# Kernel tuning notes

Hardware: AMD Instinct MI355X
Metric: run time of the kernel (lower is better)

## Reference

```python
import jax, jax.numpy as jnp
import numpy as np

N, E, D, L = 50000, 600000, 128, 3
EPS = 1e-5


def _layer_norm(x, g, b):
    m = jnp.mean(x, axis=-1, keepdims=True)
    v = jnp.mean((x - m) ** 2, axis=-1, keepdims=True)
    return (x - m) * jax.lax.rsqrt(v + EPS) * g + b


def setup_inputs() -> dict:
    key = jax.random.key(0)
    ks = jax.random.split(key, 20)
    s = 1.0 / np.sqrt(D)
    inp = {
        "node": jax.random.normal(ks[0], (N, D), jnp.float32),
        "edge_attr": jax.random.uniform(ks[1], (E,), jnp.float32),
        # stacked per-layer parameters [L, ...]
        "W_rel": jax.random.uniform(ks[2], (L, D, D), jnp.float32, -s, s),
        "b_rel": jax.random.uniform(ks[3], (L, D), jnp.float32, -s, s),
        "W_root": jax.random.uniform(ks[4], (L, D, D), jnp.float32, -s, s),
        "ln1_g": jnp.ones((L, D), jnp.float32),
        "ln1_b": jnp.zeros((L, D), jnp.float32),
        "ln2_g": jnp.ones((L, D), jnp.float32),
        "ln2_b": jnp.zeros((L, D), jnp.float32),
        "W1": jax.random.uniform(ks[5], (L, D, D), jnp.float32, -s, s),
        "b1": jax.random.uniform(ks[6], (L, D), jnp.float32, -s, s),
        "W2": jax.random.uniform(ks[7], (L, D, D), jnp.float32, -s, s),
        "b2": jax.random.uniform(ks[8], (L, D), jnp.float32, -s, s),
        "jk_W": jax.random.uniform(ks[9], (L * D, D), jnp.float32, -1.0 / np.sqrt(L * D), 1.0 / np.sqrt(L * D)),
        "jk_b": jax.random.uniform(ks[10], (D,), jnp.float32, -1.0 / np.sqrt(L * D), 1.0 / np.sqrt(L * D)),
        "edge_index": jax.random.randint(ks[11], (2, E), 0, N, jnp.int64),
        "batch_ptr": jnp.sort(jax.random.randint(ks[12], (51,), 0, N, jnp.int64)),
    }
    return inp


def reference(node, edge_attr, W_rel, b_rel, W_root, ln1_g, ln1_b, ln2_g, ln2_b,
              W1, b1, W2, b2, jk_W, jk_b, edge_index, batch_ptr):
    src, dst = edge_index[0], edge_index[1]
    deg = jax.ops.segment_sum(jnp.ones((E,), node.dtype), dst, num_segments=N)
    inv_deg = 1.0 / jnp.maximum(deg, 1.0)  # nodes with no in-edges -> 0 aggregate
    outs = []
    for l in range(L):
        msg = node[src] * edge_attr[:, None]                       # [E, D] gather
        agg = jax.ops.segment_sum(msg, dst, num_segments=N)        # scatter-sum
        mean = agg * inv_deg[:, None]                              # mean aggregation
        # GraphConv: lin_rel(aggr) + lin_root(x); skip_connection=False
        node = mean @ W_rel[l] + b_rel[l] + node @ W_root[l]
        node = jax.nn.relu(_layer_norm(node @ W1[l] + b1[l], ln1_g[l], ln1_b[l]))
        node = jax.nn.relu(_layer_norm(node @ W2[l] + b2[l], ln2_g[l], ln2_b[l]))
        outs.append(node)
    jk = jnp.concatenate(outs, axis=-1)                            # [N, L*D]
    return jk @ jk_W + jk_b
```

## Files before the change

kernel.cpp:

```cpp
#include <hip/hip_runtime.h>

#define NN 50000
#define EE 600000
#define DD 128
#define CAP 64
#define CNTSTRIDE 16
#define LDS_STRIDE 136

typedef __attribute__((ext_vector_type(8))) short bf16x8;
typedef __attribute__((ext_vector_type(4))) float f32x4;

__device__ __forceinline__ unsigned short f2bf(float f) {
    union { float f; unsigned u; } v; v.f = f;
    unsigned r = v.u + 0x7FFF + ((v.u >> 16) & 1);
    return (unsigned short)(r >> 16);
}
__device__ __forceinline__ float bflo(unsigned x) { return __uint_as_float(x << 16); }
__device__ __forceinline__ float bfhi(unsigned x) { return __uint_as_float(x & 0xffff0000u); }

#define FILL_BLKS  2344
#define CONV_BLKS  6250
__global__ void setup_kernel(const int* __restrict__ src, const int* __restrict__ dst,
                             const float* __restrict__ ea,
                             int* __restrict__ cnt, unsigned* __restrict__ slots,
                             const float* __restrict__ nodef, unsigned short* __restrict__ node_bf,
                             const float* __restrict__ W_rel, const float* __restrict__ W_root,
                             const float* __restrict__ W1, float* __restrict__ Wc,
                             const float* __restrict__ b_rel, const float* __restrict__ b1,
                             float* __restrict__ bc) {
    int b = blockIdx.x;
    if (b < FILL_BLKS) {
        int e = b * 256 + threadIdx.x;
        if (e >= EE) return;
        int d = dst[e];
        int p = atomicAdd(&cnt[d * CNTSTRIDE], 1);
        if (p < CAP) {
            unsigned w16 = (unsigned)__float2int_rn(ea[e] * 65535.0f);
            if (w16 > 65535u) w16 = 65535u;
            slots[d * CAP + p] = ((unsigned)src[e] << 16) | w16;
        }
    } else if (b < FILL_BLKS + CONV_BLKS) {
        int i = (b - FILL_BLKS) * 256 + threadIdx.x;
        float4 v = *(const float4*)&nodef[(size_t)i * 4];
        ushort4 o;
        o.x = f2bf(v.x); o.y = f2bf(v.y); o.z = f2bf(v.z); o.w = f2bf(v.w);
        *(ushort4*)&node_bf[(size_t)i * 4] = o;
    } else if (b < FILL_BLKS + CONV_BLKS + 96) {
        int bb = b - FILL_BLKS - CONV_BLKS;
        int which = bb >> 4, part = bb & 15;
        int l = (which < 3) ? which : which - 3;
        const float* A = (which < 3) ? (W_rel + (size_t)l * 16384) : (W_root + (size_t)l * 16384);
        const float* B = W1 + (size_t)l * 16384;
        float* out = Wc + (size_t)which * 16384;
        int o = part * 1024 + threadIdx.x;
        for (int rep = 0; rep < 4; ++rep, o += 256) {
            int i = o >> 7, j = o & 127;
            float s = 0.f;
            for (int k = 0; k < 128; ++k) s = fmaf(A[i * 128 + k], B[k * 128 + j], s);
            out[o] = s;
        }
    } else {
        int l = b - FILL_BLKS - CONV_BLKS - 96;
        int j = threadIdx.x;
        if (j < 128) {
            float s = 0.f;
            for (int k = 0; k < 128; ++k)
                s = fmaf(b_rel[l * 128 + k], W1[(size_t)l * 16384 + k * 128 + j], s);
            bc[l * 128 + j] = s + b1[l * 128 + j];
        }
    }
}

__global__ void pack_w_kernel(const float* __restrict__ Wc, const float* __restrict__ W2,
                              const float* __restrict__ jkW, unsigned short* __restrict__ packed) {
    int t = blockIdx.x * 256 + threadIdx.x;
    int chunk = t >> 11;
    int r = t & 2047;
    int lane = r & 63;
    int tile = r >> 6;
    int kt = tile >> 3, nt = tile & 7;
    int quad = lane >> 4, n = lane & 15;
    const float* src;
    if (chunk < 6)       src = Wc  + (size_t)chunk * 16384;
    else if (chunk < 9)  src = W2  + (size_t)(chunk - 6) * 16384;
    else                 src = jkW + (size_t)(chunk - 9) * 16384;
    int k0 = kt * 32 + quad * 8;
    int col = nt * 16 + n;
    union { unsigned short u[8]; uint4 v; } tmp;
#pragma unroll
    for (int j = 0; j < 8; ++j) tmp.u[j] = f2bf(src[(size_t)(k0 + j) * DD + col]);
    *(uint4*)&packed[(size_t)t * 8] = tmp.v;
}

__global__ __launch_bounds__(256) void gather_mean_kernel(
    const unsigned short* __restrict__ feat,
    const unsigned* __restrict__ slots,
    const int* __restrict__ cnt,
    unsigned short* __restrict__ mean) {
    const int node = (int)((blockIdx.x * 256 + threadIdx.x) >> 6);
    if (node >= NN) return;
    const int lane = threadIdx.x & 63;
    const int g  = lane >> 4;
    const int h8 = (lane & 15) * 8;
    int c = cnt[node * CNTSTRIDE];
    if (c > CAP) c = CAP;
    const unsigned* sp = slots + (size_t)node * CAP;

    float acc[8] = {0.f, 0.f, 0.f, 0.f, 0.f, 0.f, 0.f, 0.f};
    const float wscale = 1.0f / 65535.0f;

    for (int j0 = 0; j0 < c; j0 += 16) {
        uint4 sv = *(const uint4*)&sp[j0 + g * 4];
        unsigned se[4] = {sv.x, sv.y, sv.z, sv.w};
#pragma unroll
        for (int t = 0; t < 4; ++t) {
            int idx = j0 + g * 4 + t;
            bool ok = idx < c;
            unsigned e = se[t];
            int   srcn = ok ? (int)(e >> 16) : 0;
            float w    = ok ? (float)(e & 0xffffu) * wscale : 0.0f;
            uint4 v = *(const uint4*)&feat[(size_t)srcn * DD + h8];
            acc[0] = fmaf(bflo(v.x), w, acc[0]);
            acc[1] = fmaf(bfhi(v.x), w, acc[1]);
            acc[2] = fmaf(bflo(v.y), w, acc[2]);
            acc[3] = fmaf(bfhi(v.y), w, acc[3]);
            acc[4] = fmaf(bflo(v.z), w, acc[4]);
            acc[5] = fmaf(bfhi(v.z), w, acc[5]);
            acc[6] = fmaf(bflo(v.w), w, acc[6]);
            acc[7] = fmaf(bfhi(v.w), w, acc[7]);
        }
    }

#pragma unroll
    for (int k = 0; k < 8; ++k) {
        acc[k] += __shfl_xor(acc[k], 16);
        acc[k] += __shfl_xor(acc[k], 32);
    }

    if (g == 0) {
        float id = 1.0f / fmaxf((float)c, 1.0f);
        union { unsigned short u[8]; uint4 v; } o;
#pragma unroll
        for (int k = 0; k < 8; ++k) o.u[k] = f2bf(acc[k] * id);
        *(uint4*)&mean[(size_t)node * DD + h8] = o.v;
    }
}

template <bool JK>
__global__ __launch_bounds__(256) void fused_layer(
    const unsigned short* __restrict__ mean, const unsigned short* __restrict__ nodef,
    const unsigned short* __restrict__ PWrel, const unsigned short* __restrict__ PWroot,
    const unsigned short* __restrict__ PW2,
    const float* __restrict__ bc, const float* __restrict__ ln1g, const float* __restrict__ ln1b,
    const float* __restrict__ b2, const float* __restrict__ ln2g, const float* __restrict__ ln2b,
    unsigned short* __restrict__ out,
    const unsigned short* __restrict__ o0, const unsigned short* __restrict__ o1,
    const unsigned short* __restrict__ PJ0, const unsigned short* __restrict__ PJ1,
    const unsigned short* __restrict__ PJ2,
    const float* __restrict__ jkb, float* __restrict__ fout) {
    __shared__ unsigned short relay[4][16 * LDS_STRIDE];
    const int lane = threadIdx.x & 63;
    const int wid  = threadIdx.x >> 6;
    const int mrow = blockIdx.x * 64 + wid * 16;
    if (mrow >= NN) return;

    const int quad = lane >> 4, n15 = lane & 15;
    const int kq   = quad * 8;
    unsigned short* wt = relay[wid];

    const unsigned short* Am = mean  + (size_t)(mrow + n15) * DD;
    const unsigned short* An = nodef + (size_t)(mrow + n15) * DD;

    f32x4 acc[8];
#pragma unroll
    for (int nt = 0; nt < 8; ++nt) acc[nt] = (f32x4){0.f, 0.f, 0.f, 0.f};
#pragma unroll
    for (int kt = 0; kt < 4; ++kt) {
        bf16x8 am = *(const bf16x8*)&Am[kt * 32 + kq];
        bf16x8 an = *(const bf16x8*)&An[kt * 32 + kq];
#pragma unroll
        for (int nt = 0; nt < 8; ++nt) {
            bf16x8 brel = *(const bf16x8*)&PWrel[(size_t)((kt * 8 + nt) * 64 + lane) * 8];
            acc[nt] = __builtin_amdgcn_mfma_f32_16x16x32_bf16(am, brel, acc[nt], 0, 0, 0);
            bf16x8 brt = *(const bf16x8*)&PWroot[(size_t)((kt * 8 + nt) * 64 + lane) * 8];
            acc[nt] = __builtin_amdgcn_mfma_f32_16x16x32_bf16(an, brt, acc[nt], 0, 0, 0);
        }
    }

    float x[8][4];
#pragma unroll
    for (int nt = 0; nt < 8; ++nt) {
        float bv = bc[nt * 16 + n15];
#pragma unroll
        for (int r = 0; r < 4; ++r) x[nt][r] = acc[nt][r] + bv;
    }
    {
        float s[4] = {0, 0, 0, 0}, q[4] = {0, 0, 0, 0};
#pragma unroll
        for (int nt = 0; nt < 8; ++nt)
#pragma unroll
            for (int r = 0; r < 4; ++r) { s[r] += x[nt][r]; q[r] += x[nt][r] * x[nt][r]; }
#pragma unroll
        for (int m = 1; m <= 8; m <<= 1)
#pragma unroll
            for (int r = 0; r < 4; ++r) { s[r] += __shfl_xor(s[r], m); q[r] += __shfl_xor(q[r], m); }
        const float inv = 1.0f / 128.0f;
#pragma unroll
        for (int r = 0; r < 4; ++r) {
            float mu = s[r] * inv;
            float rs = rsqrtf(fmaxf(q[r] * inv - mu * mu, 0.0f) + 1e-5f);
#pragma unroll
            for (int nt = 0; nt < 8; ++nt) {
                float g = ln1g[nt * 16 + n15], bb = ln1b[nt * 16 + n15];
                x[nt][r] = fmaxf((x[nt][r] - mu) * rs * g + bb, 0.0f);
            }
        }
    }

#pragma unroll
    for (int nt = 0; nt < 8; ++nt)
#pragma unroll
        for (int r = 0; r < 4; ++r)
            wt[(quad * 4 + r) * LDS_STRIDE + nt * 16 + n15] = f2bf(x[nt][r]);
    __asm__ __volatile__("s_waitcnt lgkmcnt(0)" ::: "memory");

    f32x4 acc2[8];
#pragma unroll
    for (int nt = 0; nt < 8; ++nt) acc2[nt] = (f32x4){0.f, 0.f, 0.f, 0.f};
#pragma unroll
    for (int kt = 0; kt < 4; ++kt) {
        bf16x8 ah = *(const bf16x8*)&wt[n15 * LDS_STRIDE + kt * 32 + kq];
#pragma unroll
        for (int nt = 0; nt < 8; ++nt) {
            bf16x8 bw = *(const bf16x8*)&PW2[(size_t)((kt * 8 + nt) * 64 + lane) * 8];
            acc2[nt] = __builtin_amdgcn_mfma_f32_16x16x32_bf16(ah, bw, acc2[nt], 0, 0, 0);
        }
    }
#pragma unroll
    for (int nt = 0; nt < 8; ++nt) {
        float bv = b2[nt * 16 + n15];
#pragma unroll
        for (int r = 0; r < 4; ++r) x[nt][r] = acc2[nt][r] + bv;
    }
    {
        float s[4] = {0, 0, 0, 0}, q[4] = {0, 0, 0, 0};
#pragma unroll
        for (int nt = 0; nt < 8; ++nt)
#pragma unroll
            for (int r = 0; r < 4; ++r) { s[r] += x[nt][r]; q[r] += x[nt][r] * x[nt][r]; }
#pragma unroll
        for (int m = 1; m <= 8; m <<= 1)
#pragma unroll
            for (int r = 0; r < 4; ++r) { s[r] += __shfl_xor(s[r], m); q[r] += __shfl_xor(q[r], m); }
        const float inv = 1.0f / 128.0f;
#pragma unroll
        for (int r = 0; r < 4; ++r) {
            float mu = s[r] * inv;
            float rs = rsqrtf(fmaxf(q[r] * inv - mu * mu, 0.0f) + 1e-5f);
#pragma unroll
            for (int nt = 0; nt < 8; ++nt) {
                float g = ln2g[nt * 16 + n15], bb = ln2b[nt * 16 + n15];
                x[nt][r] = fmaxf((x[nt][r] - mu) * rs * g + bb, 0.0f);
            }
        }
    }

    __asm__ __volatile__("s_waitcnt lgkmcnt(0)" ::: "memory");
#pragma unroll
    for (int nt = 0; nt < 8; ++nt)
#pragma unroll
        for (int r = 0; r < 4; ++r)
            wt[(quad * 4 + r) * LDS_STRIDE + nt * 16 + n15] = f2bf(x[nt][r]);
    __asm__ __volatile__("s_waitcnt lgkmcnt(0)" ::: "memory");

    if constexpr (!JK) {
#pragma unroll
        for (int i = 0; i < 4; ++i) {
            int s = i * 512 + lane * 8;
            int r = s >> 7, col = s & 127;
            uint4 v = *(const uint4*)&wt[r * LDS_STRIDE + col];
            *(uint4*)&out[(size_t)(mrow + r) * DD + col] = v;
        }
    } else {
        f32x4 accJ[8];
#pragma unroll
        for (int nt = 0; nt < 8; ++nt) accJ[nt] = (f32x4){0.f, 0.f, 0.f, 0.f};
#pragma unroll
        for (int kt = 0; kt < 4; ++kt) {
            bf16x8 ah = *(const bf16x8*)&wt[n15 * LDS_STRIDE + kt * 32 + kq];
#pragma unroll
            for (int nt = 0; nt < 8; ++nt) {
                bf16x8 bw = *(const bf16x8*)&PJ2[(size_t)((kt * 8 + nt) * 64 + lane) * 8];
                accJ[nt] = __builtin_amdgcn_mfma_f32_16x16x32_bf16(ah, bw, accJ[nt], 0, 0, 0);
            }
        }
        const unsigned short* A0 = o0 + (size_t)(mrow + n15) * DD;
        const unsigned short* A1 = o1 + (size_t)(mrow + n15) * DD;
#pragma unroll
        for (int kt = 0; kt < 4; ++kt) {
            bf16x8 a0 = *(const bf16x8*)&A0[kt * 32 + kq];
            bf16x8 a1 = *(const bf16x8*)&A1[kt * 32 + kq];
#pragma unroll
            for (int nt = 0; nt < 8; ++nt) {
                bf16x8 b0 = *(const bf16x8*)&PJ0[(size_t)((kt * 8 + nt) * 64 + lane) * 8];
                accJ[nt] = __builtin_amdgcn_mfma_f32_16x16x32_bf16(a0, b0, accJ[nt], 0, 0, 0);
                bf16x8 b1 = *(const bf16x8*)&PJ1[(size_t)((kt * 8 + nt) * 64 + lane) * 8];
                accJ[nt] = __builtin_amdgcn_mfma_f32_16x16x32_bf16(a1, b1, accJ[nt], 0, 0, 0);
            }
        }
#pragma unroll
        for (int nt = 0; nt < 8; ++nt) {
            float bv = jkb[nt * 16 + n15];
#pragma unroll
            for (int r = 0; r < 4; ++r)
                fout[(size_t)(mrow + quad * 4 + r) * DD + nt * 16 + n15] = accJ[nt][r] + bv;
        }
    }
}

extern "C" void kernel_launch(void* const* d_in, const int* in_sizes, int n_in,
                              void* d_out, int out_size, void* d_ws, size_t ws_size,
                              hipStream_t stream) {
    const float* node   = (const float*)d_in[0];
    const float* ea     = (const float*)d_in[1];
    const float* W_rel  = (const float*)d_in[2];
    const float* b_rel  = (const float*)d_in[3];
    const float* W_root = (const float*)d_in[4];
    const float* ln1_g  = (const float*)d_in[5];
    const float* ln1_b  = (const float*)d_in[6];
    const float* ln2_g  = (const float*)d_in[7];
    const float* ln2_b  = (const float*)d_in[8];
    const float* W1     = (const float*)d_in[9];
    const float* b1     = (const float*)d_in[10];
    const float* W2     = (const float*)d_in[11];
    const float* b2     = (const float*)d_in[12];
    const float* jk_W   = (const float*)d_in[13];
    const float* jk_b   = (const float*)d_in[14];
    const int*   ei     = (const int*)d_in[15];
    const int* srcI = ei;
    const int* dstI = ei + EE;

    char* ws = (char*)d_ws;
    size_t off = 0;
    auto alloc = [&](size_t bytes) {
        void* p = ws + off;
        off += (bytes + 255) & ~(size_t)255;
        return p;
    };
    int*            cnt     = (int*)alloc((size_t)NN * CNTSTRIDE * 4);
    unsigned*       slots   = (unsigned*)alloc((size_t)NN * CAP * 4);
    unsigned short* node_bf = (unsigned short*)alloc((size_t)NN * DD * 2);
    unsigned short* mean_bf = (unsigned short*)alloc((size_t)NN * DD * 2);
    unsigned short* outs_bf[2];
    for (int l = 0; l < 2; ++l) outs_bf[l] = (unsigned short*)alloc((size_t)NN * DD * 2);
    float*          Wc      = (float*)alloc((size_t)6 * 16384 * 4);
    float*          bc      = (float*)alloc((size_t)3 * 128 * 4);
    unsigned short* packed  = (unsigned short*)alloc((size_t)12 * 16384 * 2);

    hipMemsetAsync(cnt, 0, (size_t)NN * CNTSTRIDE * 4, stream);
    setup_kernel<<<FILL_BLKS + CONV_BLKS + 96 + 3, 256, 0, stream>>>(
        srcI, dstI, ea, cnt, slots, node, node_bf, W_rel, W_root, W1, Wc, b_rel, b1, bc);
    pack_w_kernel<<<12 * 2048 / 256, 256, 0, stream>>>(Wc, W2, jk_W, packed);

    const int gblocks = (NN + 63) / 64;
    unsigned short* cur = node_bf;
    for (int l = 0; l < 3; ++l) {
        gather_mean_kernel<<<NN / 4, 256, 0, stream>>>(cur, slots, cnt, mean_bf);
        if (l < 2) {
            fused_layer<false><<<gblocks, 256, 0, stream>>>(
                mean_bf, cur,
                packed + (size_t)l * 16384, packed + (size_t)(3 + l) * 16384,
                packed + (size_t)(6 + l) * 16384,
                bc + (size_t)l * DD, ln1_g + (size_t)l * DD, ln1_b + (size_t)l * DD,
                b2 + (size_t)l * DD, ln2_g + (size_t)l * DD, ln2_b + (size_t)l * DD,
                outs_bf[l],
                nullptr, nullptr, nullptr, nullptr, nullptr, nullptr, nullptr);
            cur = outs_bf[l];
        } else {
            fused_layer<true><<<gblocks, 256, 0, stream>>>(
                mean_bf, cur,
                packed + (size_t)l * 16384, packed + (size_t)(3 + l) * 16384,
                packed + (size_t)(6 + l) * 16384,
                bc + (size_t)l * DD, ln1_g + (size_t)l * DD, ln1_b + (size_t)l * DD,
                b2 + (size_t)l * DD, ln2_g + (size_t)l * DD, ln2_b + (size_t)l * DD,
                nullptr,
                outs_bf[0], outs_bf[1],
                packed + (size_t)9 * 16384, packed + (size_t)10 * 16384, packed + (size_t)11 * 16384,
                jk_b, (float*)d_out);
        }
    }
}
```

Measured before the change: 304.8 us.

## Process 32 rows per wave in fused layer and prefetch gather slot indices

```diff
diff --git a/kernel.cpp b/kernel.cpp
--- a/kernel.cpp
+++ b/kernel.cpp
@@ -109,8 +109,9 @@
     float acc[8] = {0.f, 0.f, 0.f, 0.f, 0.f, 0.f, 0.f, 0.f};
     const float wscale = 1.0f / 65535.0f;
 
+    uint4 sv = *(const uint4*)&sp[g * 4];
     for (int j0 = 0; j0 < c; j0 += 16) {
-        uint4 sv = *(const uint4*)&sp[j0 + g * 4];
+        uint4 svn = (j0 + 16 < c) ? *(const uint4*)&sp[j0 + 16 + g * 4] : sv;
         unsigned se[4] = {sv.x, sv.y, sv.z, sv.w};
 #pragma unroll
         for (int t = 0; t < 4; ++t) {
@@ -129,6 +130,7 @@
             acc[6] = fmaf(bflo(v.w), w, acc[6]);
             acc[7] = fmaf(bfhi(v.w), w, acc[7]);
         }
+        sv = svn;
     }
 
 #pragma unroll
@@ -147,7 +149,7 @@
 }
 
 template <bool JK>
-__global__ __launch_bounds__(256) void fused_layer(
+__global__ __launch_bounds__(128) void fused_layer(
     const unsigned short* __restrict__ mean, const unsigned short* __restrict__ nodef,
     const unsigned short* __restrict__ PWrel, const unsigned short* __restrict__ PWroot,
     const unsigned short* __restrict__ PW2,
@@ -158,162 +160,177 @@
     const unsigned short* __restrict__ PJ0, const unsigned short* __restrict__ PJ1,
     const unsigned short* __restrict__ PJ2,
     const float* __restrict__ jkb, float* __restrict__ fout) {
-    __shared__ unsigned short relay[4][16 * LDS_STRIDE];
+    __shared__ unsigned short relay[2][32 * LDS_STRIDE];
     const int lane = threadIdx.x & 63;
     const int wid  = threadIdx.x >> 6;
-    const int mrow = blockIdx.x * 64 + wid * 16;
+    const int mrow = blockIdx.x * 64 + wid * 32;
     if (mrow >= NN) return;
+    const bool alive1 = (mrow + 16) < NN;
 
     const int quad = lane >> 4, n15 = lane & 15;
     const int kq   = quad * 8;
     unsigned short* wt = relay[wid];
 
-    const unsigned short* Am = mean  + (size_t)(mrow + n15) * DD;
-    const unsigned short* An = nodef + (size_t)(mrow + n15) * DD;
-
-    f32x4 acc[8];
-#pragma unroll
-    for (int nt = 0; nt < 8; ++nt) acc[nt] = (f32x4){0.f, 0.f, 0.f, 0.f};
+    const unsigned short* Am0 = mean  + (size_t)(mrow + n15) * DD;
+    const unsigned short* An0 = nodef + (size_t)(mrow + n15) * DD;
+    const unsigned short* Am1 = Am0 + 16 * DD;
+    const unsigned short* An1 = An0 + 16 * DD;
+
+    f32x4 acc0[8], acc1[8];
+#pragma unroll
+    for (int nt = 0; nt < 8; ++nt) { acc0[nt] = (f32x4){0,0,0,0}; acc1[nt] = (f32x4){0,0,0,0}; }
 #pragma unroll
     for (int kt = 0; kt < 4; ++kt) {
-        bf16x8 am = *(const bf16x8*)&Am[kt * 32 + kq];
-        bf16x8 an = *(const bf16x8*)&An[kt * 32 + kq];
+        bf16x8 am0 = *(const bf16x8*)&Am0[kt * 32 + kq];
+        bf16x8 an0 = *(const bf16x8*)&An0[kt * 32 + kq];
+        bf16x8 am1 = *(const bf16x8*)&Am1[kt * 32 + kq];
+        bf16x8 an1 = *(const bf16x8*)&An1[kt * 32 + kq];
 #pragma unroll
         for (int nt = 0; nt < 8; ++nt) {
             bf16x8 brel = *(const bf16x8*)&PWrel[(size_t)((kt * 8 + nt) * 64 + lane) * 8];
-            acc[nt] = __builtin_amdgcn_mfma_f32_16x16x32_bf16(am, brel, acc[nt], 0, 0, 0);
+            acc0[nt] = __builtin_amdgcn_mfma_f32_16x16x32_bf16(am0, brel, acc0[nt], 0, 0, 0);
+            acc1[nt] = __builtin_amdgcn_mfma_f32_16x16x32_bf16(am1, brel, acc1[nt], 0, 0, 0);
             bf16x8 brt = *(const bf16x8*)&PWroot[(size_t)((kt * 8 + nt) * 64 + lane) * 8];
-            acc[nt] = __builtin_amdgcn_mfma_f32_16x16x32_bf16(an, brt, acc[nt], 0, 0, 0);
-        }
-    }
-
-    float x[8][4];
-#pragma unroll
-    for (int nt = 0; nt < 8; ++nt) {
-        float bv = bc[nt * 16 + n15];
-#pragma unroll
-        for (int r = 0; r < 4; ++r) x[nt][r] = acc[nt][r] + bv;
-    }
-    {
-        float s[4] = {0, 0, 0, 0}, q[4] = {0, 0, 0, 0};
+            acc0[nt] = __builtin_amdgcn_mfma_f32_16x16x32_bf16(an0, brt, acc0[nt], 0, 0, 0);
+            acc1[nt] = __builtin_amdgcn_mfma_f32_16x16x32_bf16(an1, brt, acc1[nt], 0, 0, 0);
+        }
+    }
+
+#pragma unroll
+    for (int s = 0; s < 2; ++s) {
+        f32x4* acc = s ? acc1 : acc0;
+        float x[8][4];
+#pragma unroll
+        for (int nt = 0; nt < 8; ++nt) {
+            float bv = bc[nt * 16 + n15];
+#pragma unroll
+            for (int r = 0; r < 4; ++r) x[nt][r] = acc[nt][r] + bv;
+        }
+        float sm[4] = {0,0,0,0}, q[4] = {0,0,0,0};
 #pragma unroll
         for (int nt = 0; nt < 8; ++nt)
 #pragma unroll
-            for (int r = 0; r < 4; ++r) { s[r] += x[nt][r]; q[r] += x[nt][r] * x[nt][r]; }
+            for (int r = 0; r < 4; ++r) { sm[r] += x[nt][r]; q[r] += x[nt][r] * x[nt][r]; }
 #pragma unroll
         for (int m = 1; m <= 8; m <<= 1)
 #pragma unroll
-            for (int r = 0; r < 4; ++r) { s[r] += __shfl_xor(s[r], m); q[r] += __shfl_xor(q[r], m); }
+            for (int r = 0; r < 4; ++r) { sm[r] += __shfl_xor(sm[r], m); q[r] += __shfl_xor(q[r], m); }
         const float inv = 1.0f / 128.0f;
 #pragma unroll
         for (int r = 0; r < 4; ++r) {
-            float mu = s[r] * inv;
+            float mu = sm[r] * inv;
             float rs = rsqrtf(fmaxf(q[r] * inv - mu * mu, 0.0f) + 1e-5f);
 #pragma unroll
             for (int nt = 0; nt < 8; ++nt) {
                 float g = ln1g[nt * 16 + n15], bb = ln1b[nt * 16 + n15];
-                x[nt][r] = fmaxf((x[nt][r] - mu) * rs * g + bb, 0.0f);
-            }
-        }
-    }
-
-#pragma unroll
-    for (int nt = 0; nt < 8; ++nt)
-#pragma unroll
-        for (int r = 0; r < 4; ++r)
-            wt[(quad * 4 + r) * LDS_STRIDE + nt * 16 + n15] = f2bf(x[nt][r]);
+                wt[(s * 16 + quad * 4 + r) * LDS_STRIDE + nt * 16 + n15] =
+                    f2bf(fmaxf((x[nt][r] - mu) * rs * g + bb, 0.0f));
+            }
+        }
+    }
     __asm__ __volatile__("s_waitcnt lgkmcnt(0)" ::: "memory");
 
-    f32x4 acc2[8];
-#pragma unroll
-    for (int nt = 0; nt < 8; ++nt) acc2[nt] = (f32x4){0.f, 0.f, 0.f, 0.f};
+#pragma unroll
+    for (int nt = 0; nt < 8; ++nt) { acc0[nt] = (f32x4){0,0,0,0}; acc1[nt] = (f32x4){0,0,0,0}; }
 #pragma unroll
     for (int kt = 0; kt < 4; ++kt) {
-        bf16x8 ah = *(const bf16x8*)&wt[n15 * LDS_STRIDE + kt * 32 + kq];
+        bf16x8 ah0 = *(const bf16x8*)&wt[n15 * LDS_STRIDE + kt * 32 + kq];
+        bf16x8 ah1 = *(const bf16x8*)&wt[(16 + n15) * LDS_STRIDE + kt * 32 + kq];
 #pragma unroll
         for (int nt = 0; nt < 8; ++nt) {
             bf16x8 bw = *(const bf16x8*)&PW2[(size_t)((kt * 8 + nt) * 64 + lane) * 8];
-            acc2[nt] = __builtin_amdgcn_mfma_f32_16x16x32_bf16(ah, bw, acc2[nt], 0, 0, 0);
-        }
-    }
-#pragma unroll
-    for (int nt = 0; nt < 8; ++nt) {
-        float bv = b2[nt * 16 + n15];
-#pragma unroll
-        for (int r = 0; r < 4; ++r) x[nt][r] = acc2[nt][r] + bv;
-    }
-    {
-        float s[4] = {0, 0, 0, 0}, q[4] = {0, 0, 0, 0};
+            acc0[nt] = __builtin_amdgcn_mfma_f32_16x16x32_bf16(ah0, bw, acc0[nt], 0, 0, 0);
+            acc1[nt] = __builtin_amdgcn_mfma_f32_16x16x32_bf16(ah1, bw, acc1[nt], 0, 0, 0);
+        }
+    }
+    __asm__ __volatile__("s_waitcnt lgkmcnt(0)" ::: "memory");
+
+#pragma unroll
+    for (int s = 0; s < 2; ++s) {
+        f32x4* acc = s ? acc1 : acc0;
+        float x[8][4];
+#pragma unroll
+        for (int nt = 0; nt < 8; ++nt) {
+            float bv = b2[nt * 16 + n15];
+#pragma unroll
+            for (int r = 0; r < 4; ++r) x[nt][r] = acc[nt][r] + bv;
+        }
+        float sm[4] = {0,0,0,0}, q[4] = {0,0,0,0};
 #pragma unroll
         for (int nt = 0; nt < 8; ++nt)
 #pragma unroll
-            for (int r = 0; r < 4; ++r) { s[r] += x[nt][r]; q[r] += x[nt][r] * x[nt][r]; }
+            for (int r = 0; r < 4; ++r) { sm[r] += x[nt][r]; q[r] += x[nt][r] * x[nt][r]; }
 #pragma unroll
         for (int m = 1; m <= 8; m <<= 1)
 #pragma unroll
-            for (int r = 0; r < 4; ++r) { s[r] += __shfl_xor(s[r], m); q[r] += __shfl_xor(q[r], m); }
+            for (int r = 0; r < 4; ++r) { sm[r] += __shfl_xor(sm[r], m); q[r] += __shfl_xor(q[r], m); }
         const float inv = 1.0f / 128.0f;
 #pragma unroll
         for (int r = 0; r < 4; ++r) {
-            float mu = s[r] * inv;
+            float mu = sm[r] * inv;
             float rs = rsqrtf(fmaxf(q[r] * inv - mu * mu, 0.0f) + 1e-5f);
 #pragma unroll
             for (int nt = 0; nt < 8; ++nt) {
                 float g = ln2g[nt * 16 + n15], bb = ln2b[nt * 16 + n15];
-                x[nt][r] = fmaxf((x[nt][r] - mu) * rs * g + bb, 0.0f);
-            }
-        }
-    }
-
+                wt[(s * 16 + quad * 4 + r) * LDS_STRIDE + nt * 16 + n15] =
+                    f2bf(fmaxf((x[nt][r] - mu) * rs * g + bb, 0.0f));
+            }
+        }
+    }
     __asm__ __volatile__("s_waitcnt lgkmcnt(0)" ::: "memory");
-#pragma unroll
-    for (int nt = 0; nt < 8; ++nt)
-#pragma unroll
-        for (int r = 0; r < 4; ++r)
-            wt[(quad * 4 + r) * LDS_STRIDE + nt * 16 + n15] = f2bf(x[nt][r]);
-    __asm__ __volatile__("s_waitcnt lgkmcnt(0)" ::: "memory");
 
     if constexpr (!JK) {
 #pragma unroll
-        for (int i = 0; i < 4; ++i) {
+        for (int i = 0; i < 8; ++i) {
             int s = i * 512 + lane * 8;
             int r = s >> 7, col = s & 127;
-            uint4 v = *(const uint4*)&wt[r * LDS_STRIDE + col];
-            *(uint4*)&out[(size_t)(mrow + r) * DD + col] = v;
+            if (mrow + r < NN) {
+                uint4 v = *(const uint4*)&wt[r * LDS_STRIDE + col];
+                *(uint4*)&out[(size_t)(mrow + r) * DD + col] = v;
+            }
         }
     } else {
-        f32x4 accJ[8];
-#pragma unroll
-        for (int nt = 0; nt < 8; ++nt) accJ[nt] = (f32x4){0.f, 0.f, 0.f, 0.f};
+        f32x4 accJ0[8], accJ1[8];
+#pragma unroll
+        for (int nt = 0; nt < 8; ++nt) { accJ0[nt] = (f32x4){0,0,0,0}; accJ1[nt] = (f32x4){0,0,0,0}; }
 #pragma unroll
         for (int kt = 0; kt < 4; ++kt) {
-            bf16x8 ah = *(const bf16x8*)&wt[n15 * LDS_STRIDE + kt * 32 + kq];
+            bf16x8 ah0 = *(const bf16x8*)&wt[n15 * LDS_STRIDE + kt * 32 + kq];
+            bf16x8 ah1 = *(const bf16x8*)&wt[(16 + n15) * LDS_STRIDE + kt * 32 + kq];
 #pragma unroll
             for (int nt = 0; nt < 8; ++nt) {
                 bf16x8 bw = *(const bf16x8*)&PJ2[(size_t)((kt * 8 + nt) * 64 + lane) * 8];
-                accJ[nt] = __builtin_amdgcn_mfma_f32_16x16x32_bf16(ah, bw, accJ[nt], 0, 0, 0);
-            }
-        }
-        const unsigned short* A0 = o0 + (size_t)(mrow + n15) * DD;
-        const unsigned short* A1 = o1 + (size_t)(mrow + n15) * DD;
+                accJ0[nt] = __builtin_amdgcn_mfma_f32_16x16x32_bf16(ah0, bw, accJ0[nt], 0, 0, 0);
+                accJ1[nt] = __builtin_amdgcn_mfma_f32_16x16x32_bf16(ah1, bw, accJ1[nt], 0, 0, 0);
+            }
+        }
+        const unsigned short* A00 = o0 + (size_t)(mrow + n15) * DD;
+        const unsigned short* A10 = o1 + (size_t)(mrow + n15) * DD;
 #pragma unroll
         for (int kt = 0; kt < 4; ++kt) {
-            bf16x8 a0 = *(const bf16x8*)&A0[kt * 32 + kq];
-            bf16x8 a1 = *(const bf16x8*)&A1[kt * 32 + kq];
+            bf16x8 a00 = *(const bf16x8*)&A00[kt * 32 + kq];
+            bf16x8 a01 = *(const bf16x8*)&A00[16 * DD + kt * 32 + kq];
+            bf16x8 a10 = *(const bf16x8*)&A10[kt * 32 + kq];
+            bf16x8 a11 = *(const bf16x8*)&A10[16 * DD + kt * 32 + kq];
 #pragma unroll
             for (int nt = 0; nt < 8; ++nt) {
                 bf16x8 b0 = *(const bf16x8*)&PJ0[(size_t)((kt * 8 + nt) * 64 + lane) * 8];
-                accJ[nt] = __builtin_amdgcn_mfma_f32_16x16x32_bf16(a0, b0, accJ[nt], 0, 0, 0);
+                accJ0[nt] = __builtin_amdgcn_mfma_f32_16x16x32_bf16(a00, b0, accJ0[nt], 0, 0, 0);
+                accJ1[nt] = __builtin_amdgcn_mfma_f32_16x16x32_bf16(a01, b0, accJ1[nt], 0, 0, 0);
                 bf16x8 b1 = *(const bf16x8*)&PJ1[(size_t)((kt * 8 + nt) * 64 + lane) * 8];
-                accJ[nt] = __builtin_amdgcn_mfma_f32_16x16x32_bf16(a1, b1, accJ[nt], 0, 0, 0);
+                accJ0[nt] = __builtin_amdgcn_mfma_f32_16x16x32_bf16(a10, b1, accJ0[nt], 0, 0, 0);
+                accJ1[nt] = __builtin_amdgcn_mfma_f32_16x16x32_bf16(a11, b1, accJ1[nt], 0, 0, 0);
             }
         }
 #pragma unroll
         for (int nt = 0; nt < 8; ++nt) {
             float bv = jkb[nt * 16 + n15];
 #pragma unroll
-            for (int r = 0; r < 4; ++r)
-                fout[(size_t)(mrow + quad * 4 + r) * DD + nt * 16 + n15] = accJ[nt][r] + bv;
+            for (int r = 0; r < 4; ++r) {
+                fout[(size_t)(mrow + quad * 4 + r) * DD + nt * 16 + n15] = accJ0[nt][r] + bv;
+                if (alive1)
+                    fout[(size_t)(mrow + 16 + quad * 4 + r) * DD + nt * 16 + n15] = accJ1[nt][r] + bv;
+            }
         }
     }
 }
@@ -356,6 +373,7 @@
     float*          Wc      = (float*)alloc((size_t)6 * 16384 * 4);
     float*          bc      = (float*)alloc((size_t)3 * 128 * 4);
     unsigned short* packed  = (unsigned short*)alloc((size_t)12 * 16384 * 2);
+    (void)alloc((size_t)64 * DD * 2);
 
     hipMemsetAsync(cnt, 0, (size_t)NN * CNTSTRIDE * 4, stream);
     setup_kernel<<<FILL_BLKS + CONV_BLKS + 96 + 3, 256, 0, stream>>>(
@@ -367,7 +385,7 @@
     for (int l = 0; l < 3; ++l) {
         gather_mean_kernel<<<NN / 4, 256, 0, stream>>>(cur, slots, cnt, mean_bf);
         if (l < 2) {
-            fused_layer<false><<<gblocks, 256, 0, stream>>>(
+            fused_layer<false><<<gblocks, 128, 0, stream>>>(
                 mean_bf, cur,
                 packed + (size_t)l * 16384, packed + (size_t)(3 + l) * 16384,
                 packed + (size_t)(6 + l) * 16384,
@@ -377,7 +395,7 @@
                 nullptr, nullptr, nullptr, nullptr, nullptr, nullptr, nullptr);
             cur = outs_bf[l];
         } else {
-            fused_layer<true><<<gblocks, 256, 0, stream>>>(
+            fused_layer<true><<<gblocks, 128, 0, stream>>>(
                 mean_bf, cur,
                 packed + (size_t)l * 16384, packed + (size_t)(3 + l) * 16384,
                 packed + (size_t)(6 + l) * 16384,
```

Measured after the change: 391.0 us. +28.3%, slower.

## Fuse neighbor gather-mean into the per-layer fused MLP kernel

Applied to the files above, without the earlier changes.

```diff
diff --git a/kernel.cpp b/kernel.cpp
--- a/kernel.cpp
+++ b/kernel.cpp
@@ -92,63 +92,10 @@
     *(uint4*)&packed[(size_t)t * 8] = tmp.v;
 }
 
-__global__ __launch_bounds__(256) void gather_mean_kernel(
-    const unsigned short* __restrict__ feat,
-    const unsigned* __restrict__ slots,
-    const int* __restrict__ cnt,
-    unsigned short* __restrict__ mean) {
-    const int node = (int)((blockIdx.x * 256 + threadIdx.x) >> 6);
-    if (node >= NN) return;
-    const int lane = threadIdx.x & 63;
-    const int g  = lane >> 4;
-    const int h8 = (lane & 15) * 8;
-    int c = cnt[node * CNTSTRIDE];
-    if (c > CAP) c = CAP;
-    const unsigned* sp = slots + (size_t)node * CAP;
-
-    float acc[8] = {0.f, 0.f, 0.f, 0.f, 0.f, 0.f, 0.f, 0.f};
-    const float wscale = 1.0f / 65535.0f;
-
-    for (int j0 = 0; j0 < c; j0 += 16) {
-        uint4 sv = *(const uint4*)&sp[j0 + g * 4];
-        unsigned se[4] = {sv.x, sv.y, sv.z, sv.w};
-#pragma unroll
-        for (int t = 0; t < 4; ++t) {
-            int idx = j0 + g * 4 + t;
-            bool ok = idx < c;
-            unsigned e = se[t];
-            int   srcn = ok ? (int)(e >> 16) : 0;
-            float w    = ok ? (float)(e & 0xffffu) * wscale : 0.0f;
-            uint4 v = *(const uint4*)&feat[(size_t)srcn * DD + h8];
-            acc[0] = fmaf(bflo(v.x), w, acc[0]);
-            acc[1] = fmaf(bfhi(v.x), w, acc[1]);
-            acc[2] = fmaf(bflo(v.y), w, acc[2]);
-            acc[3] = fmaf(bfhi(v.y), w, acc[3]);
-            acc[4] = fmaf(bflo(v.z), w, acc[4]);
-            acc[5] = fmaf(bfhi(v.z), w, acc[5]);
-            acc[6] = fmaf(bflo(v.w), w, acc[6]);
-            acc[7] = fmaf(bfhi(v.w), w, acc[7]);
-        }
-    }
-
-#pragma unroll
-    for (int k = 0; k < 8; ++k) {
-        acc[k] += __shfl_xor(acc[k], 16);
-        acc[k] += __shfl_xor(acc[k], 32);
-    }
-
-    if (g == 0) {
-        float id = 1.0f / fmaxf((float)c, 1.0f);
-        union { unsigned short u[8]; uint4 v; } o;
-#pragma unroll
-        for (int k = 0; k < 8; ++k) o.u[k] = f2bf(acc[k] * id);
-        *(uint4*)&mean[(size_t)node * DD + h8] = o.v;
-    }
-}
-
 template <bool JK>
 __global__ __launch_bounds__(256) void fused_layer(
-    const unsigned short* __restrict__ mean, const unsigned short* __restrict__ nodef,
+    const unsigned short* __restrict__ feat,
+    const unsigned* __restrict__ slots, const int* __restrict__ cnt,
     const unsigned short* __restrict__ PWrel, const unsigned short* __restrict__ PWroot,
     const unsigned short* __restrict__ PW2,
     const float* __restrict__ bc, const float* __restrict__ ln1g, const float* __restrict__ ln1b,
@@ -158,7 +105,8 @@
     const unsigned short* __restrict__ PJ0, const unsigned short* __restrict__ PJ1,
     const unsigned short* __restrict__ PJ2,
     const float* __restrict__ jkb, float* __restrict__ fout) {
-    __shared__ unsigned short relay[4][16 * LDS_STRIDE];
+    __shared__ unsigned short gtile[4][16 * LDS_STRIDE];
+    __shared__ uint4 slds[4][16][4];
     const int lane = threadIdx.x & 63;
     const int wid  = threadIdx.x >> 6;
     const int mrow = blockIdx.x * 64 + wid * 16;
@@ -166,17 +114,90 @@
 
     const int quad = lane >> 4, n15 = lane & 15;
     const int kq   = quad * 8;
-    unsigned short* wt = relay[wid];
-
-    const unsigned short* Am = mean  + (size_t)(mrow + n15) * DD;
-    const unsigned short* An = nodef + (size_t)(mrow + n15) * DD;
+    const int g    = quad;
+    const int h8   = n15 * 8;
+    unsigned short* wt = gtile[wid];
+
+    {
+        int nslot = mrow + (lane >> 2); if (nslot > NN - 1) nslot = NN - 1;
+        slds[wid][lane >> 2][lane & 3] =
+            *(const uint4*)&slots[(size_t)nslot * CAP + (lane & 3) * 4];
+        int ncnt = mrow + n15; if (ncnt > NN - 1) ncnt = NN - 1;
+        int cv = cnt[(size_t)ncnt * CNTSTRIDE];
+        __asm__ __volatile__("s_waitcnt lgkmcnt(0)" ::: "memory");
+        const float wscale = 1.0f / 65535.0f;
+#pragma unroll
+        for (int i = 0; i < 16; ++i) {
+            int c = __shfl(cv, i);
+            if (c > CAP) c = CAP;
+            float acc[8] = {0.f, 0.f, 0.f, 0.f, 0.f, 0.f, 0.f, 0.f};
+            uint4 se = slds[wid][i][g];
+            unsigned ses[4] = {se.x, se.y, se.z, se.w};
+#pragma unroll
+            for (int t = 0; t < 4; ++t) {
+                int idx = g * 4 + t;
+                bool ok = idx < c;
+                unsigned e = ses[t];
+                int   srcn = ok ? (int)(e >> 16) : 0;
+                float w    = ok ? (float)(e & 0xffffu) * wscale : 0.0f;
+                uint4 v = *(const uint4*)&feat[(size_t)srcn * DD + h8];
+                acc[0] = fmaf(bflo(v.x), w, acc[0]);
+                acc[1] = fmaf(bfhi(v.x), w, acc[1]);
+                acc[2] = fmaf(bflo(v.y), w, acc[2]);
+                acc[3] = fmaf(bfhi(v.y), w, acc[3]);
+                acc[4] = fmaf(bflo(v.z), w, acc[4]);
+                acc[5] = fmaf(bfhi(v.z), w, acc[5]);
+                acc[6] = fmaf(bflo(v.w), w, acc[6]);
+                acc[7] = fmaf(bfhi(v.w), w, acc[7]);
+            }
+            if (c > 16) {
+                const unsigned* sp = slots + (size_t)(mrow + i) * CAP;
+                for (int j0 = 16; j0 < c; j0 += 16) {
+                    uint4 s2 = *(const uint4*)&sp[j0 + g * 4];
+                    unsigned s2s[4] = {s2.x, s2.y, s2.z, s2.w};
+#pragma unroll
+                    for (int t = 0; t < 4; ++t) {
+                        int idx = j0 + g * 4 + t;
+                        bool ok = idx < c;
+                        unsigned e = s2s[t];
+                        int   srcn = ok ? (int)(e >> 16) : 0;
+                        float w    = ok ? (float)(e & 0xffffu) * wscale : 0.0f;
+                        uint4 v = *(const uint4*)&feat[(size_t)srcn * DD + h8];
+                        acc[0] = fmaf(bflo(v.x), w, acc[0]);
+                        acc[1] = fmaf(bfhi(v.x), w, acc[1]);
+                        acc[2] = fmaf(bflo(v.y), w, acc[2]);
+                        acc[3] = fmaf(bfhi(v.y), w, acc[3]);
+                        acc[4] = fmaf(bflo(v.z), w, acc[4]);
+                        acc[5] = fmaf(bfhi(v.z), w, acc[5]);
+                        acc[6] = fmaf(bflo(v.w), w, acc[6]);
+                        acc[7] = fmaf(bfhi(v.w), w, acc[7]);
+                    }
+                }
+            }
+#pragma unroll
+            for (int k = 0; k < 8; ++k) {
+                acc[k] += __shfl_xor(acc[k], 16);
+                acc[k] += __shfl_xor(acc[k], 32);
+            }
+            if (g == 0) {
+                float id = 1.0f / fmaxf((float)c, 1.0f);
+                union { unsigned short u[8]; uint4 v; } o;
+#pragma unroll
+                for (int k = 0; k < 8; ++k) o.u[k] = f2bf(acc[k] * id);
+                *(uint4*)&wt[i * LDS_STRIDE + h8] = o.v;
+            }
+        }
+        __asm__ __volatile__("s_waitcnt lgkmcnt(0)" ::: "memory");
+    }
+
+    const unsigned short* An = feat + (size_t)(mrow + n15) * DD;
 
     f32x4 acc[8];
 #pragma unroll
     for (int nt = 0; nt < 8; ++nt) acc[nt] = (f32x4){0.f, 0.f, 0.f, 0.f};
 #pragma unroll
     for (int kt = 0; kt < 4; ++kt) {
-        bf16x8 am = *(const bf16x8*)&Am[kt * 32 + kq];
+        bf16x8 am = *(const bf16x8*)&wt[n15 * LDS_STRIDE + kt * 32 + kq];
         bf16x8 an = *(const bf16x8*)&An[kt * 32 + kq];
 #pragma unroll
         for (int nt = 0; nt < 8; ++nt) {
@@ -211,8 +232,8 @@
             float rs = rsqrtf(fmaxf(q[r] * inv - mu * mu, 0.0f) + 1e-5f);
 #pragma unroll
             for (int nt = 0; nt < 8; ++nt) {
-                float g = ln1g[nt * 16 + n15], bb = ln1b[nt * 16 + n15];
-                x[nt][r] = fmaxf((x[nt][r] - mu) * rs * g + bb, 0.0f);
+                float gg = ln1g[nt * 16 + n15], bb = ln1b[nt * 16 + n15];
+                x[nt][r] = fmaxf((x[nt][r] - mu) * rs * gg + bb, 0.0f);
             }
         }
     }
@@ -259,8 +280,8 @@
             float rs = rsqrtf(fmaxf(q[r] * inv - mu * mu, 0.0f) + 1e-5f);
 #pragma unroll
             for (int nt = 0; nt < 8; ++nt) {
-                float g = ln2g[nt * 16 + n15], bb = ln2b[nt * 16 + n15];
-                x[nt][r] = fmaxf((x[nt][r] - mu) * rs * g + bb, 0.0f);
+                float gg = ln2g[nt * 16 + n15], bb = ln2b[nt * 16 + n15];
+                x[nt][r] = fmaxf((x[nt][r] - mu) * rs * gg + bb, 0.0f);
             }
         }
     }
@@ -350,12 +371,12 @@
     int*            cnt     = (int*)alloc((size_t)NN * CNTSTRIDE * 4);
     unsigned*       slots   = (unsigned*)alloc((size_t)NN * CAP * 4);
     unsigned short* node_bf = (unsigned short*)alloc((size_t)NN * DD * 2);
-    unsigned short* mean_bf = (unsigned short*)alloc((size_t)NN * DD * 2);
     unsigned short* outs_bf[2];
     for (int l = 0; l < 2; ++l) outs_bf[l] = (unsigned short*)alloc((size_t)NN * DD * 2);
     float*          Wc      = (float*)alloc((size_t)6 * 16384 * 4);
     float*          bc      = (float*)alloc((size_t)3 * 128 * 4);
     unsigned short* packed  = (unsigned short*)alloc((size_t)12 * 16384 * 2);
+    (void)alloc((size_t)64 * DD * 4);
 
     hipMemsetAsync(cnt, 0, (size_t)NN * CNTSTRIDE * 4, stream);
     setup_kernel<<<FILL_BLKS + CONV_BLKS + 96 + 3, 256, 0, stream>>>(
@@ -365,10 +386,9 @@
     const int gblocks = (NN + 63) / 64;
     unsigned short* cur = node_bf;
     for (int l = 0; l < 3; ++l) {
-        gather_mean_kernel<<<NN / 4, 256, 0, stream>>>(cur, slots, cnt, mean_bf);
         if (l < 2) {
             fused_layer<false><<<gblocks, 256, 0, stream>>>(
-                mean_bf, cur,
+                cur, slots, cnt,
                 packed + (size_t)l * 16384, packed + (size_t)(3 + l) * 16384,
                 packed + (size_t)(6 + l) * 16384,
                 bc + (size_t)l * DD, ln1_g + (size_t)l * DD, ln1_b + (size_t)l * DD,
@@ -378,7 +398,7 @@
             cur = outs_bf[l];
         } else {
             fused_layer<true><<<gblocks, 256, 0, stream>>>(
-                mean_bf, cur,
+                cur, slots, cnt,
                 packed + (size_t)l * 16384, packed + (size_t)(3 + l) * 16384,
                 packed + (size_t)(6 + l) * 16384,
                 bc + (size_t)l * DD, ln1_g + (size_t)l * DD, ln1_b + (size_t)l * DD,
```

Result: slower. 345.5 us (+13.3%).
